# Optimization experiments

Measured on AMD Instinct MI355X. Metric: run time of the kernel, lower is better.

The kernel has to match this reference:

```python
import jax, jax.numpy as jnp
import numpy as np

N = 20000      # nodes
E = 320000     # edges (avg degree 16)
F_IN = 768
DIMS = [(768, 1536), (1536, 768), (768, 384), (384, 256), (256, 5)]


def setup_inputs() -> dict:
    key = jax.random.key(0)
    ks = jax.random.split(key, 2 + 3 * len(DIMS))
    inp = {
        'x': jax.random.normal(ks[0], (N, F_IN), dtype=jnp.float32),
        'edge_index': jax.random.randint(ks[1], (2, E), 0, N, dtype=jnp.int64),
    }
    for li, (fi, fo) in enumerate(DIMS):
        s = 1.0 / np.sqrt(fi)
        inp[f'Wl{li+1}'] = jax.random.uniform(ks[2 + 3 * li], (fi, fo), jnp.float32, -s, s)
        inp[f'Wr{li+1}'] = jax.random.uniform(ks[3 + 3 * li], (fi, fo), jnp.float32, -s, s)
        inp[f'b{li+1}'] = jax.random.uniform(ks[4 + 3 * li], (fo,), jnp.float32, -s, s)
    return inp


def _sage_conv(x, src, dst, deg_inv, Wl, Wr, b):
    # mean aggregate neighbor features, then linear (mean commutes with linear,
    # matching PyG SAGEConv which aggregates x_j then applies lin_l)
    agg = jax.ops.segment_sum(x[src], dst, num_segments=N) * deg_inv  # [N, F_in]
    return agg @ Wl + x @ Wr + b


def reference(x, edge_index,
              Wl1, Wr1, b1, Wl2, Wr2, b2, Wl3, Wr3, b3,
              Wl4, Wr4, b4, Wl5, Wr5, b5):
    src, dst = edge_index[0], edge_index[1]
    deg = jax.ops.segment_sum(jnp.ones((E,), jnp.float32), dst, num_segments=N)
    deg_inv = (1.0 / jnp.maximum(deg, 1.0))[:, None]  # clamp like PyG mean aggr

    h = jax.nn.relu(_sage_conv(x, src, dst, deg_inv, Wl1, Wr1, b1))
    h = jax.nn.relu(_sage_conv(h, src, dst, deg_inv, Wl2, Wr2, b2))
    h = jax.nn.relu(_sage_conv(h, src, dst, deg_inv, Wl3, Wr3, b3))
    h = jax.nn.relu(_sage_conv(h, src, dst, deg_inv, Wl4, Wr4, b4))  # [N, 256]
    out = _sage_conv(h, src, dst, deg_inv, Wl5, Wr5, b5)             # [N, 5]
    return (h, out)
```

## Files before the change

kernel.cpp:

```cpp
#include <hip/hip_runtime.h>
#include <stdint.h>

typedef __attribute__((ext_vector_type(8))) short short8;
typedef __attribute__((ext_vector_type(4))) float f32x4;
typedef __attribute__((ext_vector_type(8))) unsigned short us8;

__device__ __forceinline__ float bf2f(unsigned short s) {
  return __uint_as_float(((unsigned)s) << 16);
}
__device__ __forceinline__ unsigned short f2bf(float f) {
  unsigned u = __float_as_uint(f);
  u += 0x7fffu + ((u >> 16) & 1u);
  return (unsigned short)(u >> 16);
}

__global__ void gs_count_deg(const int* __restrict__ dst, int* __restrict__ cnt, int E) {
  int e = blockIdx.x * 256 + threadIdx.x;
  if (e < E) atomicAdd(&cnt[dst[e]], 1);
}

__global__ void gs_scanA(const int* __restrict__ cnt, int* __restrict__ rp,
                         int* __restrict__ bsum, int n) {
  __shared__ int sm[256];
  const int b = blockIdx.x, t = threadIdx.x;
  const int base = b * 1024 + t * 4;
  int v[4]; int s = 0;
#pragma unroll
  for (int i = 0; i < 4; ++i) { v[i] = (base + i < n) ? cnt[base + i] : 0; s += v[i]; }
  sm[t] = s;
  __syncthreads();
  for (int off = 1; off < 256; off <<= 1) {
    int x = (t >= off) ? sm[t - off] : 0;
    __syncthreads();
    sm[t] += x;
    __syncthreads();
  }
  int run = sm[t] - s;
#pragma unroll
  for (int i = 0; i < 4; ++i) { if (base + i < n) rp[base + i] = run; run += v[i]; }
  if (t == 255) bsum[b] = sm[255];
}

__global__ void gs_scanB(int* bsum, int nb) {
  if (threadIdx.x == 0 && blockIdx.x == 0) {
    int run = 0;
    for (int i = 0; i < nb; ++i) { int v = bsum[i]; bsum[i] = run; run += v; }
    bsum[nb] = run;
  }
}

__global__ void gs_scanC(int* __restrict__ rp, int* __restrict__ cur,
                         const int* __restrict__ bsum, int n, int nb) {
  int i = blockIdx.x * 256 + threadIdx.x;
  if (i < n) {
    int v = rp[i] + bsum[i >> 10];
    rp[i] = v;
    cur[i] = v;
  }
  if (i == n) rp[n] = bsum[nb];
}

__global__ void gs_fill_csr(const int* __restrict__ src, const int* __restrict__ dst,
                            int* __restrict__ cur, int* __restrict__ col, int E) {
  int e = blockIdx.x * 256 + threadIdx.x;
  if (e < E) {
    int pos = atomicAdd(&cur[dst[e]], 1);
    col[pos] = src[e];
  }
}

__global__ void gs_f32_to_bf16(const float* __restrict__ in, unsigned short* __restrict__ out, int n4) {
  int i = blockIdx.x * 256 + threadIdx.x;
  if (i < n4) {
    float4 f = ((const float4*)in)[i];
    ushort4 o;
    o.x = f2bf(f.x); o.y = f2bf(f.y); o.z = f2bf(f.z); o.w = f2bf(f.w);
    ((ushort4*)out)[i] = o;
  }
}

struct TP { const float* W; unsigned short* WT; int K, F; };
struct TP8 { TP t[8]; };

__global__ void gs_tpack8(TP8 args) {
  const TP a = args.t[blockIdx.z];
  const int k0 = blockIdx.x * 32, f0 = blockIdx.y * 32;
  if (k0 >= a.K || f0 >= a.F) return;
  __shared__ float t[32][33];
  const int tx = threadIdx.x, ty = threadIdx.y;
#pragma unroll
  for (int r = ty; r < 32; r += 8) {
    int k = k0 + r, f = f0 + tx;
    t[r][tx] = (k < a.K && f < a.F) ? a.W[(size_t)k * a.F + f] : 0.f;
  }
  __syncthreads();
#pragma unroll
  for (int r = ty; r < 32; r += 8) {
    int f = f0 + r, k = k0 + tx;
    if (f < a.F && k < a.K) a.WT[(size_t)f * a.K + k] = f2bf(t[tx][r]);
  }
}

__global__ __launch_bounds__(64)
void gs_agg_wide(const unsigned short* __restrict__ C, int ldc, int zoff,
                 const int* __restrict__ rp, const int* __restrict__ col,
                 const float* __restrict__ bias,
                 unsigned short* __restrict__ hout, float* __restrict__ fout,
                 int F, int relu) {
  const int v = blockIdx.x;
  const int l = threadIdx.x;
  const int cc = blockIdx.y * 512 + 8 * l;
  const bool act = (cc < F);
  const int s0 = rp[v], s1 = rp[v + 1];
  const float inv = 1.0f / (float)max(s1 - s0, 1);
  float a[8];
#pragma unroll
  for (int k = 0; k < 8; ++k) a[k] = 0.f;

  __shared__ int nb[64];
  for (int base = s0; base < s1; base += 64) {
    int m = min(s1 - base, 64);
    __syncthreads();
    if (l < m) nb[l] = col[base + l];
    __syncthreads();
    int j = 0;
    for (; j + 4 <= m; j += 4) {
      if (act) {
        us8 u0 = *(const us8*)(C + (size_t)nb[j + 0] * ldc + cc);
        us8 u1 = *(const us8*)(C + (size_t)nb[j + 1] * ldc + cc);
        us8 u2 = *(const us8*)(C + (size_t)nb[j + 2] * ldc + cc);
        us8 u3 = *(const us8*)(C + (size_t)nb[j + 3] * ldc + cc);
#pragma unroll
        for (int k = 0; k < 8; ++k)
          a[k] += bf2f(u0[k]) + bf2f(u1[k]) + bf2f(u2[k]) + bf2f(u3[k]);
      }
    }
    for (; j < m; ++j) {
      if (act) {
        us8 u = *(const us8*)(C + (size_t)nb[j] * ldc + cc);
#pragma unroll
        for (int k = 0; k < 8; ++k) a[k] += bf2f(u[k]);
      }
    }
  }
  if (!act) return;

  float o[8];
#pragma unroll
  for (int k = 0; k < 8; ++k) o[k] = a[k] * inv;
  if (zoff >= 0) {
    us8 u = *(const us8*)(C + (size_t)v * ldc + zoff + cc);
#pragma unroll
    for (int k = 0; k < 8; ++k) o[k] += bf2f(u[k]);
  }
  if (bias) {
    float4 b0 = *(const float4*)(bias + cc);
    float4 b1 = *(const float4*)(bias + cc + 4);
    o[0] += b0.x; o[1] += b0.y; o[2] += b0.z; o[3] += b0.w;
    o[4] += b1.x; o[5] += b1.y; o[6] += b1.z; o[7] += b1.w;
  }
  if (relu) {
#pragma unroll
    for (int k = 0; k < 8; ++k) o[k] = fmaxf(o[k], 0.f);
  }
  if (hout) {
    us8 u;
#pragma unroll
    for (int k = 0; k < 8; ++k) u[k] = f2bf(o[k]);
    *(us8*)(hout + (size_t)v * F + cc) = u;
  }
  if (fout) {
    *(float4*)(fout + (size_t)v * F + cc) = make_float4(o[0], o[1], o[2], o[3]);
    *(float4*)(fout + (size_t)v * F + cc + 4) = make_float4(o[4], o[5], o[6], o[7]);
  }
}

__global__ __launch_bounds__(256)
void gs_gemm(const unsigned short* __restrict__ A1, const unsigned short* __restrict__ A2,
             const unsigned short* __restrict__ B1, const unsigned short* __restrict__ B2,
             const float* __restrict__ bias, unsigned short* __restrict__ Hout,
             int M, int Nn, int K, int doRelu, int Mt, int Nt) {
  __shared__ unsigned short lA[128 * 64];
  __shared__ unsigned short lB[128 * 64];
  const int tid = threadIdx.x;
  const int wid = tid >> 6;
  const int lane = tid & 63;

  const int MG = 8;
  const int per = MG * Nt;
  const int g = blockIdx.x / per;
  const int rem = blockIdx.x - g * per;
  const int gsz = min(MG, Mt - g * MG);
  const int nIdx = rem / gsz;
  const int mIdx = g * MG + (rem - nIdx * gsz);
  const int bM = mIdx * 128;
  const int bN = nIdx * 128;
  const int wM = (wid >> 1) * 64;
  const int wN = (wid & 1) * 64;

  f32x4 acc[4][4];
#pragma unroll
  for (int i = 0; i < 4; ++i)
#pragma unroll
    for (int j = 0; j < 4; ++j) acc[i][j] = (f32x4){0.f, 0.f, 0.f, 0.f};

  const int mrow = wM + (lane & 15);
  const int nrow = wN + (lane & 15);
  const int q = lane >> 4;
  const int swz = lane & 7;
  const int srow = wid * 8 + (lane >> 3);
  const int sc = (lane & 7) ^ (lane >> 3);
  const int npass = A2 ? 2 : 1;

  for (int pass = 0; pass < npass; ++pass) {
    const unsigned short* Ap = pass ? A2 : A1;
    const unsigned short* Bp = pass ? B2 : B1;
    for (int k0 = 0; k0 < K; k0 += 64) {
#pragma unroll
      for (int r = 0; r < 4; ++r) {
        int row = r * 32 + srow;
        int ga = bM + row;
        if (ga >= M) ga = M - 1;
        const unsigned short* gpA = Ap + (size_t)ga * K + k0 + sc * 8;
        const unsigned short* gpB = Bp + (size_t)(bN + row) * K + k0 + sc * 8;
        unsigned lo = (unsigned)(r * 32 + wid * 8) * 128;
        __builtin_amdgcn_global_load_lds(
            (const __attribute__((address_space(1))) unsigned int*)gpA,
            (__attribute__((address_space(3))) unsigned int*)((char*)lA + lo), 16, 0, 0);
        __builtin_amdgcn_global_load_lds(
            (const __attribute__((address_space(1))) unsigned int*)gpB,
            (__attribute__((address_space(3))) unsigned int*)((char*)lB + lo), 16, 0, 0);
      }
      __syncthreads();
#pragma unroll
      for (int s = 0; s < 2; ++s) {
        const int cofs = ((s * 4 + q) ^ swz) * 8;
        short8 aF[4], bF[4];
#pragma unroll
        for (int i = 0; i < 4; ++i) {
          aF[i] = *(const short8*)&lA[(mrow + i * 16) * 64 + cofs];
          bF[i] = *(const short8*)&lB[(nrow + i * 16) * 64 + cofs];
        }
#pragma unroll
        for (int i = 0; i < 4; ++i)
#pragma unroll
          for (int j = 0; j < 4; ++j)
            acc[i][j] = __builtin_amdgcn_mfma_f32_16x16x32_bf16(aF[i], bF[j], acc[i][j], 0, 0, 0);
      }
      __syncthreads();
    }
  }

  const int rbase = bM + wM + (lane >> 4) * 4;
#pragma unroll
  for (int i = 0; i < 4; ++i) {
#pragma unroll
    for (int r = 0; r < 4; ++r) {
      int row = rbase + i * 16 + r;
      if (row >= M) continue;
#pragma unroll
      for (int j = 0; j < 4; ++j) {
        int colN = bN + wN + j * 16 + (lane & 15);
        float v = acc[i][j][r];
        if (bias) v += bias[colN];
        if (doRelu) v = fmaxf(v, 0.f);
        Hout[(size_t)row * Nn + colN] = f2bf(v);
      }
    }
  }
}

__global__ __launch_bounds__(64)
void gs_l5dot(const unsigned short* __restrict__ h4, const float* __restrict__ Wl,
              const float* __restrict__ Wr, float* __restrict__ yz) {
  __shared__ float sW[2560];
  const int v = blockIdx.x;
  const int l = threadIdx.x;
  for (int i = l; i < 2560; i += 64) sW[i] = (i < 1280) ? Wl[i] : Wr[i - 1280];
  __syncthreads();
  ushort4 u = ((const ushort4*)(h4 + (size_t)v * 256))[l];
  float hv[4] = {bf2f(u.x), bf2f(u.y), bf2f(u.z), bf2f(u.w)};
  float acc[10];
#pragma unroll
  for (int n = 0; n < 10; ++n) acc[n] = 0.f;
#pragma unroll
  for (int t = 0; t < 4; ++t) {
    int k = 4 * l + t;
#pragma unroll
    for (int n = 0; n < 5; ++n) {
      acc[n] += hv[t] * sW[k * 5 + n];
      acc[5 + n] += hv[t] * sW[1280 + k * 5 + n];
    }
  }
#pragma unroll
  for (int n = 0; n < 10; ++n)
    for (int off = 32; off > 0; off >>= 1) acc[n] += __shfl_down(acc[n], off, 64);
  if (l == 0) {
#pragma unroll
    for (int n = 0; n < 10; ++n) yz[(size_t)v * 10 + n] = acc[n];
  }
}

__global__ __launch_bounds__(64)
void gs_l5agg(const float* __restrict__ yz, const int* __restrict__ rp,
              const int* __restrict__ col, const float* __restrict__ b,
              float* __restrict__ out) {
  const int v = blockIdx.x;
  const int l = threadIdx.x;
  const int s0 = rp[v], s1 = rp[v + 1];
  const float inv = 1.0f / (float)max(s1 - s0, 1);
  float acc[5] = {0.f, 0.f, 0.f, 0.f, 0.f};
  for (int e = s0 + l; e < s1; e += 64) {
    const float* yr = yz + (size_t)col[e] * 10;
#pragma unroll
    for (int n = 0; n < 5; ++n) acc[n] += yr[n];
  }
#pragma unroll
  for (int n = 0; n < 5; ++n)
    for (int off = 32; off > 0; off >>= 1) acc[n] += __shfl_down(acc[n], off, 64);
  if (l == 0) {
#pragma unroll
    for (int n = 0; n < 5; ++n)
      out[(size_t)v * 5 + n] = acc[n] * inv + yz[(size_t)v * 10 + 5 + n] + b[n];
  }
}

extern "C" void kernel_launch(void* const* d_in, const int* in_sizes, int n_in,
                              void* d_out, int out_size, void* d_ws, size_t ws_size,
                              hipStream_t stream) {
  const float* x = (const float*)d_in[0];
  const int* ei = (const int*)d_in[1];
  const int N = in_sizes[0] / 768;
  const int E = in_sizes[1] / 2;
  const int* src = ei;
  const int* dst = ei + E;

  const float* Wl[5];
  const float* Wr[5];
  const float* bb[5];
  for (int l = 0; l < 5; ++l) {
    Wl[l] = (const float*)d_in[2 + 3 * l];
    Wr[l] = (const float*)d_in[3 + 3 * l];
    bb[l] = (const float*)d_in[4 + 3 * l];
  }

  char* w = (char*)d_ws;
  size_t off = 0;
  auto take = [&](size_t bytes) -> char* {
    char* p = w + off;
    off = (off + bytes + 255) & ~(size_t)255;
    return p;
  };
  unsigned short* ar1 = (unsigned short*)take((size_t)N * 768 * 2);
  unsigned short* ar2 = (unsigned short*)take((size_t)N * 768 * 2);
  unsigned short* ar3 = (unsigned short*)take((size_t)N * 1536 * 2);
  unsigned short* C2  = (unsigned short*)take((size_t)N * 1536 * 2);
  int* cnt  = (int*)take((size_t)N * 4);
  int* rp   = (int*)take((size_t)(N + 1) * 4);
  int* cur  = (int*)take((size_t)N * 4);
  int* col  = (int*)take((size_t)E * 4);
  const int nbChunks = (N + 1023) / 1024;
  int* bsum = (int*)take((size_t)(nbChunks + 1) * 4);
  unsigned short* WT1l = (unsigned short*)take((size_t)1536 * 768 * 2);
  unsigned short* WT1r = (unsigned short*)take((size_t)1536 * 768 * 2);
  unsigned short* WT2  = (unsigned short*)take((size_t)1536 * 1536 * 2);
  unsigned short* WT3  = (unsigned short*)take((size_t)768 * 768 * 2);
  unsigned short* WT4  = (unsigned short*)take((size_t)512 * 384 * 2);

  unsigned short* xb   = ar1;
  unsigned short* C3   = ar1;
  unsigned short* aggb = ar2;
  unsigned short* h2   = ar2;
  unsigned short* h1   = ar3;
  unsigned short* C4   = ar3;
  unsigned short* h3   = ar3 + (size_t)N * 512;
  unsigned short* h4   = ar3 + (size_t)N * (512 + 384);
  float*          yz5  = (float*)(ar3 + (size_t)N * (512 + 384 + 256));

  const int M = N;
  const int Mt = (M + 127) / 128;

  hipMemsetAsync(cnt, 0, (size_t)N * 4, stream);
  gs_count_deg<<<(E + 255) / 256, 256, 0, stream>>>(dst, cnt, E);
  gs_scanA<<<nbChunks, 256, 0, stream>>>(cnt, rp, bsum, N);
  gs_scanB<<<1, 64, 0, stream>>>(bsum, nbChunks);
  gs_scanC<<<(N + 256) / 256, 256, 0, stream>>>(rp, cur, bsum, N, nbChunks);
  gs_fill_csr<<<(E + 255) / 256, 256, 0, stream>>>(src, dst, cur, col, E);

  gs_f32_to_bf16<<<((N * 768 / 4) + 255) / 256, 256, 0, stream>>>(x, xb, N * 768 / 4);
  TP8 tp;
  tp.t[0] = {Wl[0], WT1l, 768, 1536};
  tp.t[1] = {Wr[0], WT1r, 768, 1536};
  tp.t[2] = {Wl[1], WT2, 1536, 768};
  tp.t[3] = {Wr[1], WT2 + (size_t)768 * 1536, 1536, 768};
  tp.t[4] = {Wl[2], WT3, 768, 384};
  tp.t[5] = {Wr[2], WT3 + (size_t)384 * 768, 768, 384};
  tp.t[6] = {Wl[3], WT4, 384, 256};
  tp.t[7] = {Wr[3], WT4 + (size_t)256 * 384, 384, 256};
  gs_tpack8<<<dim3(48, 48, 8), dim3(32, 8), 0, stream>>>(tp);

  float* houtF = (float*)d_out;
  float* out5  = (float*)d_out + (size_t)N * 256;

  gs_agg_wide<<<dim3(N, 2), 64, 0, stream>>>(xb, 768, -1, rp, col, nullptr, aggb, nullptr, 768, 0);
  gs_gemm<<<Mt * 12, 256, 0, stream>>>(aggb, xb, WT1l, WT1r, bb[0], h1, M, 1536, 768, 1, Mt, 12);

  gs_gemm<<<Mt * 12, 256, 0, stream>>>(h1, nullptr, WT2, nullptr, nullptr, C2, M, 1536, 1536, 0, Mt, 12);
  gs_agg_wide<<<dim3(N, 2), 64, 0, stream>>>(C2, 1536, 768, rp, col, bb[1], h2, nullptr, 768, 1);

  gs_gemm<<<Mt * 6, 256, 0, stream>>>(h2, nullptr, WT3, nullptr, nullptr, C3, M, 768, 768, 0, Mt, 6);
  gs_agg_wide<<<dim3(N, 1), 64, 0, stream>>>(C3, 768, 384, rp, col, bb[2], h3, nullptr, 384, 1);

  gs_gemm<<<Mt * 4, 256, 0, stream>>>(h3, nullptr, WT4, nullptr, nullptr, C4, M, 512, 384, 0, Mt, 4);
  gs_agg_wide<<<dim3(N, 1), 64, 0, stream>>>(C4, 512, 256, rp, col, bb[3], h4, houtF, 256, 1);

  gs_l5dot<<<N, 64, 0, stream>>>(h4, Wl[4], Wr[4], yz5);
  gs_l5agg<<<N, 64, 0, stream>>>(yz5, rp, col, bb[4], out5);
}
```

Baseline: 693.2 us.

## Split neighbor aggregation across 8 edge slots per wave with shuffle reduction

The aggregation kernel now maps each 64-lane block to a 64-column slice, with 8 lanes covering the columns and 8 slots processing different neighbors in parallel. Partial sums are combined with cross-lane xor shuffles. The grid grows along the feature dimension. This is meant to fix underutilized lanes, since 384- and 256-wide layers previously left many lanes idle, and to expose more memory-level parallelism per neighbor. The cost is more blocks, redundant neighbor-index loads per column slice, and a shuffle reduction.

```diff
diff --git a/kernel.cpp b/kernel.cpp
--- a/kernel.cpp
+++ b/kernel.cpp
@@ -102,15 +102,16 @@
 }
 
 __global__ __launch_bounds__(64)
-void gs_agg_wide(const unsigned short* __restrict__ C, int ldc, int zoff,
-                 const int* __restrict__ rp, const int* __restrict__ col,
-                 const float* __restrict__ bias,
-                 unsigned short* __restrict__ hout, float* __restrict__ fout,
-                 int F, int relu) {
+void gs_agg_g8(const unsigned short* __restrict__ C, int ldc, int zoff,
+               const int* __restrict__ rp, const int* __restrict__ col,
+               const float* __restrict__ bias,
+               unsigned short* __restrict__ hout, float* __restrict__ fout,
+               int F, int relu) {
   const int v = blockIdx.x;
-  const int l = threadIdx.x;
-  const int cc = blockIdx.y * 512 + 8 * l;
-  const bool act = (cc < F);
+  const int lane = threadIdx.x;
+  const int slot = lane >> 3;
+  const int l8 = lane & 7;
+  const int cc = blockIdx.y * 64 + l8 * 8;
   const int s0 = rp[v], s1 = rp[v + 1];
   const float inv = 1.0f / (float)max(s1 - s0, 1);
   float a[8];
@@ -121,29 +122,41 @@
   for (int base = s0; base < s1; base += 64) {
     int m = min(s1 - base, 64);
     __syncthreads();
-    if (l < m) nb[l] = col[base + l];
+    if (lane < m) nb[lane] = col[base + lane];
     __syncthreads();
-    int j = 0;
-    for (; j + 4 <= m; j += 4) {
-      if (act) {
-        us8 u0 = *(const us8*)(C + (size_t)nb[j + 0] * ldc + cc);
-        us8 u1 = *(const us8*)(C + (size_t)nb[j + 1] * ldc + cc);
-        us8 u2 = *(const us8*)(C + (size_t)nb[j + 2] * ldc + cc);
-        us8 u3 = *(const us8*)(C + (size_t)nb[j + 3] * ldc + cc);
-#pragma unroll
-        for (int k = 0; k < 8; ++k)
-          a[k] += bf2f(u0[k]) + bf2f(u1[k]) + bf2f(u2[k]) + bf2f(u3[k]);
+    int iters = (m + 7) >> 3;
+    int it = 0;
+    for (; it + 2 <= iters; it += 2) {
+      int e0 = it * 8 + slot, e1 = e0 + 8;
+      bool p0 = e0 < m, p1 = e1 < m;
+      us8 u0, u1;
+      if (p0) u0 = *(const us8*)(C + (size_t)nb[e0] * ldc + cc);
+      if (p1) u1 = *(const us8*)(C + (size_t)nb[e1] * ldc + cc);
+      if (p0) {
+#pragma unroll
+        for (int k = 0; k < 8; ++k) a[k] += bf2f(u0[k]);
+      }
+      if (p1) {
+#pragma unroll
+        for (int k = 0; k < 8; ++k) a[k] += bf2f(u1[k]);
       }
     }
-    for (; j < m; ++j) {
-      if (act) {
-        us8 u = *(const us8*)(C + (size_t)nb[j] * ldc + cc);
+    for (; it < iters; ++it) {
+      int e = it * 8 + slot;
+      if (e < m) {
+        us8 u = *(const us8*)(C + (size_t)nb[e] * ldc + cc);
 #pragma unroll
         for (int k = 0; k < 8; ++k) a[k] += bf2f(u[k]);
       }
     }
   }
-  if (!act) return;
+
+#pragma unroll
+  for (int off = 8; off < 64; off <<= 1) {
+#pragma unroll
+    for (int k = 0; k < 8; ++k) a[k] += __shfl_xor(a[k], off, 64);
+  }
+  if (slot != 0) return;
 
   float o[8];
 #pragma unroll
@@ -402,17 +415,17 @@
   float* houtF = (float*)d_out;
   float* out5  = (float*)d_out + (size_t)N * 256;
 
-  gs_agg_wide<<<dim3(N, 2), 64, 0, stream>>>(xb, 768, -1, rp, col, nullptr, aggb, nullptr, 768, 0);
+  gs_agg_g8<<<dim3(N, 12), 64, 0, stream>>>(xb, 768, -1, rp, col, nullptr, aggb, nullptr, 768, 0);
   gs_gemm<<<Mt * 12, 256, 0, stream>>>(aggb, xb, WT1l, WT1r, bb[0], h1, M, 1536, 768, 1, Mt, 12);
 
   gs_gemm<<<Mt * 12, 256, 0, stream>>>(h1, nullptr, WT2, nullptr, nullptr, C2, M, 1536, 1536, 0, Mt, 12);
-  gs_agg_wide<<<dim3(N, 2), 64, 0, stream>>>(C2, 1536, 768, rp, col, bb[1], h2, nullptr, 768, 1);
+  gs_agg_g8<<<dim3(N, 12), 64, 0, stream>>>(C2, 1536, 768, rp, col, bb[1], h2, nullptr, 768, 1);
 
   gs_gemm<<<Mt * 6, 256, 0, stream>>>(h2, nullptr, WT3, nullptr, nullptr, C3, M, 768, 768, 0, Mt, 6);
-  gs_agg_wide<<<dim3(N, 1), 64, 0, stream>>>(C3, 768, 384, rp, col, bb[2], h3, nullptr, 384, 1);
+  gs_agg_g8<<<dim3(N, 6), 64, 0, stream>>>(C3, 768, 384, rp, col, bb[2], h3, nullptr, 384, 1);
 
   gs_gemm<<<Mt * 4, 256, 0, stream>>>(h3, nullptr, WT4, nullptr, nullptr, C4, M, 512, 384, 0, Mt, 4);
-  gs_agg_wide<<<dim3(N, 1), 64, 0, stream>>>(C4, 512, 256, rp, col, bb[3], h4, houtF, 256, 1);
+  gs_agg_g8<<<dim3(N, 4), 64, 0, stream>>>(C4, 512, 256, rp, col, bb[3], h4, houtF, 256, 1);
 
   gs_l5dot<<<N, 64, 0, stream>>>(h4, Wl[4], Wr[4], yz5);
   gs_l5agg<<<N, 64, 0, stream>>>(yz5, rp, col, bb[4], out5);
```

Result: slower. 761.2 us (+9.8%).
